# Optimization experiments

Measured on AMD Instinct MI355X. Metric: run time of the kernel, lower is better.

The kernel has to match this reference:

```python
import jax, jax.numpy as jnp
import numpy as np

NSAMPLE = 1024   # FPS centroids S
NGROUP = 32      # neighbors per ball K
RADIUS = 0.2


def _sqdist(a, b):
    # a: [B,S,3], b: [B,N,3] -> [B,S,N] squared euclidean distances
    return (jnp.sum(a * a, -1)[:, :, None]
            + jnp.sum(b * b, -1)[:, None, :]
            - 2.0 * jnp.einsum('bsc,bnc->bsn', a, b))


def farthest_point_sample(xyz, npoint):
    # xyz: [B,N,3] -> indices [B,npoint]. Deterministic start at index 0
    # (torch version randomizes the first centroid).
    B, N, _ = xyz.shape

    def step(carry, _):
        distance, farthest = carry
        centroid = jnp.take_along_axis(xyz, farthest[:, None, None], axis=1)  # [B,1,3]
        d = jnp.sum((xyz - centroid) ** 2, -1)                                 # [B,N]
        distance = jnp.minimum(distance, d)
        new_far = jnp.argmax(distance, -1).astype(jnp.int32)
        return (distance, new_far), farthest

    init = (jnp.full((B, N), 1e10, xyz.dtype), jnp.zeros((B,), jnp.int32))
    _, cents = jax.lax.scan(step, init, None, length=npoint)  # [npoint,B]
    return cents.T  # [B,npoint]


def query_ball_point(radius, nsample, xyz, new_xyz):
    # xyz: [B,N,3], new_xyz: [B,S,3] -> int idx [B,S,nsample]
    B, N, _ = xyz.shape
    sqr = _sqdist(new_xyz, xyz)                       # [B,S,N]
    idx = jnp.broadcast_to(jnp.arange(N, dtype=jnp.int32), sqr.shape)
    idx = jnp.where(sqr > radius * radius, N, idx)    # invalid -> sentinel N
    idx = jnp.sort(idx, axis=-1)[:, :, :nsample]      # smallest valid indices first
    first = idx[:, :, :1]
    idx = jnp.where(idx == N, first, idx)             # pad with first neighbor
    return idx.astype(jnp.int32)


def _gather_points(points, idx):
    # points: [B,N,C], idx: [B,S,K] -> [B,S,K,C]
    return jax.vmap(lambda p, i: p[i])(points, idx)


def setup_inputs() -> dict:
    key = jax.random.key(0)
    ks = jax.random.split(key, 8)
    B, N, D = 16, 8192, 64
    xyz = jax.random.uniform(ks[0], (B, N, 3), dtype=jnp.float32)
    points_fea = jax.random.normal(ks[1], (B, N, D), dtype=jnp.float32)
    s = 0.05
    W1 = jax.random.normal(ks[2], (67, 64), dtype=jnp.float32) * s
    b1 = jnp.zeros((64,), jnp.float32)
    W2 = jax.random.normal(ks[3], (64, 128), dtype=jnp.float32) * s
    b2 = jnp.zeros((128,), jnp.float32)
    W3 = jax.random.normal(ks[4], (128, 256), dtype=jnp.float32) * s
    b3 = jnp.zeros((256,), jnp.float32)
    return {"xyz": xyz, "points_fea": points_fea, "W1": W1, "b1": b1,
            "W2": W2, "b2": b2, "W3": W3, "b3": b3}


def reference(xyz, points_fea, W1, b1, W2, b2, W3, b3):
    # --- sample_and_group (fps + ball query) ---
    fps_idx = farthest_point_sample(xyz, NSAMPLE)                       # [B,S]
    sampled_xyz = jnp.take_along_axis(xyz, fps_idx[..., None], axis=1)  # [B,S,3]
    grouped_idx = query_ball_point(RADIUS, NGROUP, xyz, sampled_xyz)    # [B,S,K]
    grouped_xyz = _gather_points(xyz, grouped_idx)                      # [B,S,K,3]
    rel = grouped_xyz - sampled_xyz[:, :, None, :]
    grouped_fea = _gather_points(points_fea, grouped_idx)               # [B,S,K,D]
    feats = jnp.concatenate([rel, grouped_fea], axis=-1)                # [B,S,K,3+D]
    # --- per-point MLP (Linear+ReLU x3) ---
    h = jax.nn.relu(feats @ W1 + b1)
    h = jax.nn.relu(h @ W2 + b2)
    h = jax.nn.relu(h @ W3 + b3)                                        # [B,S,K,256]
    # --- max-pool over neighbors ---
    out = jnp.max(h, axis=2)                                            # [B,S,256]
    return sampled_xyz, out
```

## Files before the change

### kernel.cpp

```cpp
#include <hip/hip_runtime.h>
#include <hip/hip_bf16.h>

#define N_PTS 8192
#define NSAMP 1024
#define NGRP  32

typedef __attribute__((ext_vector_type(8))) short bf16x8;
typedef __attribute__((ext_vector_type(4))) float f32x4;
typedef __attribute__((ext_vector_type(2))) float f32x2;

static __device__ inline unsigned short f2bf(float f) {
  __hip_bfloat16 h = __float2bfloat16(f);
  return __builtin_bit_cast(unsigned short, h);
}

#define DPP_MAXSTEP(r, ctrl)                                                  \
  r = fmaxf(r, __int_as_float(__builtin_amdgcn_update_dpp(                    \
          __float_as_int(r), __float_as_int(r), (ctrl), 0xf, 0xf, false)))

#define FINAL8(P, V, F) do {                                                  \
    const uint4* pp_ = (const uint4*)&(P)[0];                                 \
    uint4 p0_ = pp_[0], p1_ = pp_[1], p2_ = pp_[2], p3_ = pp_[3];             \
    V = __uint_as_float(p0_.x); F = p0_.y;                                    \
    float q_;                                                                 \
    q_ = __uint_as_float(p0_.z); if (q_ > V) { V = q_; F = p0_.w; }           \
    q_ = __uint_as_float(p1_.x); if (q_ > V) { V = q_; F = p1_.y; }           \
    q_ = __uint_as_float(p1_.z); if (q_ > V) { V = q_; F = p1_.w; }           \
    q_ = __uint_as_float(p2_.x); if (q_ > V) { V = q_; F = p2_.y; }           \
    q_ = __uint_as_float(p2_.z); if (q_ > V) { V = q_; F = p2_.w; }           \
    q_ = __uint_as_float(p3_.x); if (q_ > V) { V = q_; F = p3_.y; }           \
    q_ = __uint_as_float(p3_.z); if (q_ > V) { V = q_; F = p3_.w; }           \
  } while (0)

static __device__ inline void load16(const float* __restrict__ bx, int t,
                                     float px[16], float py[16], float pz[16]) {
  const float4* src = (const float4*)(bx + t * 48);
  float4 v0 = src[0], v1 = src[1], v2 = src[2];
  float4 v3 = src[3], v4 = src[4], v5 = src[5];
  float4 v6 = src[6], v7 = src[7], v8 = src[8];
  float4 v9 = src[9], v10 = src[10], v11 = src[11];
  px[ 0]=v0.x; py[ 0]=v0.y; pz[ 0]=v0.z;
  px[ 1]=v0.w; py[ 1]=v1.x; pz[ 1]=v1.y;
  px[ 2]=v1.z; py[ 2]=v1.w; pz[ 2]=v2.x;
  px[ 3]=v2.y; py[ 3]=v2.z; pz[ 3]=v2.w;
  px[ 4]=v3.x; py[ 4]=v3.y; pz[ 4]=v3.z;
  px[ 5]=v3.w; py[ 5]=v4.x; pz[ 5]=v4.y;
  px[ 6]=v4.z; py[ 6]=v4.w; pz[ 6]=v5.x;
  px[ 7]=v5.y; py[ 7]=v5.z; pz[ 7]=v5.w;
  px[ 8]=v6.x; py[ 8]=v6.y; pz[ 8]=v6.z;
  px[ 9]=v6.w; py[ 9]=v7.x; pz[ 9]=v7.y;
  px[10]=v7.z; py[10]=v7.w; pz[10]=v8.x;
  px[11]=v8.y; py[11]=v8.z; pz[11]=v8.w;
  px[12]=v9.x; py[12]=v9.y; pz[12]=v9.z;
  px[13]=v9.w; py[13]=v10.x; pz[13]=v10.y;
  px[14]=v10.z; py[14]=v10.w; pz[14]=v11.x;
  px[15]=v11.y; py[15]=v11.z; pz[15]=v11.w;
}

__global__
__attribute__((amdgpu_flat_work_group_size(512, 512)))
__attribute__((amdgpu_waves_per_eu(2, 2)))
void fps_kernel(
    const float* __restrict__ xyz, float* __restrict__ out_sampled)
{
  #pragma clang fp contract(off)
  const int b = blockIdx.x;
  const int t = threadIdx.x;
  const float* bx = xyz + (size_t)b * N_PTS * 3;

  float px[16], py[16], pz[16];
  load16(bx, t, px, py, pz);

  f32x2 px2[8], py2[8], pz2[8], ds2[8];
  #pragma unroll
  for (int j = 0; j < 8; ++j) {
    px2[j] = (f32x2){px[2*j], px[2*j+1]};
    py2[j] = (f32x2){py[2*j], py[2*j+1]};
    pz2[j] = (f32x2){pz[2*j], pz[2*j+1]};
    ds2[j] = (f32x2){10000000000.0f, 10000000000.0f};
  }

  __shared__ float lds_p[N_PTS * 3];
  __shared__ float out_lds[NSAMP * 3];
  __shared__ __align__(16) uint2 part[2][8];

  for (int i = t; i < N_PTS * 3; i += 512) lds_p[i] = bx[i];

  const int lane = t & 63;
  const int wv   = t >> 6;

  float cx = bx[0], cy = bx[1], cz = bx[2];

  for (int it = 0; it < NSAMP; ++it) {
    if (t == 0) {
      out_lds[it * 3 + 0] = cx;
      out_lds[it * 3 + 1] = cy;
      out_lds[it * 3 + 2] = cz;
    }

    const f32x2 c2x = (f32x2){cx, cx};
    const f32x2 c2y = (f32x2){cy, cy};
    const f32x2 c2z = (f32x2){cz, cz};
    f32x2 bv2 = (f32x2){-1.0f, -1.0f};
    #pragma unroll
    for (int j = 0; j < 8; ++j) {
      f32x2 dx = px2[j] - c2x;
      f32x2 dy = py2[j] - c2y;
      f32x2 dz = pz2[j] - c2z;
      f32x2 d  = __builtin_elementwise_fma(
          dz, dz, __builtin_elementwise_fma(dy, dy, dx * dx));
      f32x2 nd = __builtin_elementwise_min(ds2[j], d);
      ds2[j] = nd;
      bv2 = __builtin_elementwise_max(bv2, nd);
    }
    float bv = fmaxf(bv2.x, bv2.y);

    int bi = t * 16 + 15;
    #pragma unroll
    for (int r = 14; r >= 0; --r) {
      float dr = (r & 1) ? ds2[r >> 1].y : ds2[r >> 1].x;
      bi = (dr == bv) ? (t * 16 + r) : bi;
    }

    float rmax = bv;
    DPP_MAXSTEP(rmax, 0x111);
    DPP_MAXSTEP(rmax, 0x112);
    DPP_MAXSTEP(rmax, 0x114);
    DPP_MAXSTEP(rmax, 0x118);
    DPP_MAXSTEP(rmax, 0x142);
    DPP_MAXSTEP(rmax, 0x143);
    float vmax = __int_as_float(
        __builtin_amdgcn_readlane(__float_as_int(rmax), 63));

    unsigned long long m = __ballot(bv == vmax);
    int L = __ffsll((long long)m) - 1;
    int widx = __builtin_amdgcn_readlane(bi, L);

    const int slot = it & 1;
    if (lane == 0) part[slot][wv] = make_uint2(__float_as_uint(vmax), (unsigned)widx);
    __syncthreads();

    float v; unsigned f;
    FINAL8(part[slot], v, f);

    cx = lds_p[f * 3 + 0];
    cy = lds_p[f * 3 + 1];
    cz = lds_p[f * 3 + 2];
  }

  __syncthreads();
  float* ob = out_sampled + (size_t)b * NSAMP * 3;
  for (int i = t; i < NSAMP * 3; i += 512) ob[i] = out_lds[i];
}

__global__ __launch_bounds__(256) void ball_kernel(
    const float* __restrict__ xyz, const float* __restrict__ sampled,
    int* __restrict__ gidx)
{
  #pragma clang fp contract(off)
  const float R2 = (float)(0.2 * 0.2);
  int gt = blockIdx.x * 256 + threadIdx.x;
  int w = gt >> 6;
  int lane = gt & 63;
  const int b = w >> 10;
  const float* cp = sampled + (size_t)w * 3;
  float cx = cp[0], cy = cp[1], cz = cp[2];
  float na = ((cx * cx) + (cy * cy)) + (cz * cz);
  const float* bx = xyz + (size_t)b * N_PTS * 3;
  int* out = gidx + (size_t)w * NGRP;

  int cnt = 0;
  int first = 0;
  for (int base = 0; base < N_PTS && cnt < NGRP; base += 64) {
    int p = base + lane;
    float x = bx[p * 3 + 0];
    float y = bx[p * 3 + 1];
    float z = bx[p * 3 + 2];
    float nb  = ((x * x) + (y * y)) + (z * z);
    float dot = fmaf(cz, z, fmaf(cy, y, cx * x));
    float sq  = (na + nb) - (2.0f * dot);
    bool inr = !(sq > R2);
    unsigned long long m = __ballot(inr);
    if (cnt == 0 && m != 0ull) first = base + (__ffsll(m) - 1);
    int before = __popcll(m & ((1ull << lane) - 1ull));
    int pos = cnt + before;
    if (inr && pos < NGRP) out[pos] = p;
    cnt += __popcll(m);
  }
  if (cnt < NGRP) {
    int q = cnt + lane;
    if (q < NGRP) out[q] = first;
  }
}

__global__ __launch_bounds__(256) void prep_w_kernel(
    const float* __restrict__ W1, const float* __restrict__ W2,
    const float* __restrict__ W3, unsigned short* __restrict__ wf1,
    unsigned short* __restrict__ wf2, unsigned short* __restrict__ wf3)
{
  int tid = blockIdx.x * 256 + threadIdx.x;
  int rec = tid >> 6, lane = tid & 63;
  if (rec >= 92) return;
  const float* W; unsigned short* dst; int N, K, ksteps, rl; int permuted;
  if (rec < 12)      { W = W1; dst = wf1; N = 64;  K = 67;  ksteps = 3; rl = rec;     permuted = 1; }
  else if (rec < 28) { W = W2; dst = wf2; N = 128; K = 64;  ksteps = 2; rl = rec - 12; permuted = 0; }
  else               { W = W3; dst = wf3; N = 256; K = 128; ksteps = 4; rl = rec - 28; permuted = 0; }
  int nt = rl / ksteps, ks = rl - nt * ksteps;
  int n  = nt * 16 + (lane & 15);
  int kb = ks * 32 + (lane >> 4) * 8;
  unsigned short v[8] __attribute__((aligned(16)));
  #pragma unroll
  for (int j = 0; j < 8; ++j) {
    int k = kb + j;
    float val;
    if (permuted) {
      if (k < 64)      val = W[(k + 3) * N + n];
      else if (k < K)  val = W[(k - 64) * N + n];
      else             val = 0.0f;
    } else {
      val = (k < K) ? W[k * N + n] : 0.0f;
    }
    v[j] = f2bf(val);
  }
  *(uint4*)(dst + ((size_t)rl * 64 + lane) * 8) = *(const uint4*)v;
}

__global__ __launch_bounds__(256, 4) void mlp_mfma_kernel(
    const float* __restrict__ xyz, const float* __restrict__ fea,
    const float* __restrict__ sampled, const int* __restrict__ gidx,
    const unsigned short* __restrict__ wf1, const unsigned short* __restrict__ wf2,
    const unsigned short* __restrict__ wf3, const float* __restrict__ b1,
    const float* __restrict__ b2, const float* __restrict__ b3,
    float* __restrict__ out)
{
  __shared__ __align__(16) unsigned short fT[32][104];
  __shared__ __align__(16) unsigned short h1[32][72];
  __shared__ __align__(16) unsigned short h2[32][136];
  __shared__ float pmax[8][256];
  __shared__ int   sidx[32];
  __shared__ float sc[4];

  const int bs = blockIdx.x;
  const int b  = bs >> 10;
  const int t  = threadIdx.x;
  const int w    = t >> 6;
  const int lane = t & 63;
  const int quad = lane >> 4;
  const int ncol = lane & 15;

  if (t < 32) sidx[t] = gidx[(size_t)bs * 32 + t];
  if (t < 3)  sc[t] = sampled[(size_t)bs * 3 + t];
  __syncthreads();

  {
    const int pt = t >> 3, c0 = t & 7;
    const int p = sidx[pt];
    const float4* fp4 = (const float4*)(fea + ((size_t)b * N_PTS + p) * 64);

    float4 fa = fp4[c0];
    float4 fb = fp4[c0 + 8];
    unsigned short sa[4] __attribute__((aligned(8)));
    unsigned short sb[4] __attribute__((aligned(8)));
    sa[0] = f2bf(fa.x); sa[1] = f2bf(fa.y); sa[2] = f2bf(fa.z); sa[3] = f2bf(fa.w);
    sb[0] = f2bf(fb.x); sb[1] = f2bf(fb.y); sb[2] = f2bf(fb.z); sb[3] = f2bf(fb.w);
    *(uint2*)&fT[pt][c0 * 4]      = *(const uint2*)sa;
    *(uint2*)&fT[pt][32 + c0 * 4] = *(const uint2*)sb;

    if (c0 == 0) {
      const float* xp = xyz + ((size_t)b * N_PTS + p) * 3;
      unsigned short sr[4] __attribute__((aligned(8)));
      sr[0] = f2bf(xp[0] - sc[0]);
      sr[1] = f2bf(xp[1] - sc[1]);
      sr[2] = f2bf(xp[2] - sc[2]);
      sr[3] = 0;
      *(uint2*)&fT[pt][64] = *(const uint2*)sr;
      *(uint2*)&fT[pt][68] = (uint2){0u, 0u};
    } else if (c0 >= 4 && c0 <= 6) {
      *(uint4*)&fT[pt][72 + (c0 - 4) * 8] = (uint4){0u, 0u, 0u, 0u};
    }
  }
  __syncthreads();

  #pragma unroll
  for (int q2 = 0; q2 < 2; ++q2) {
    const int tid = w * 2 + q2, mt = tid & 1, nt = tid >> 1;
    float bb = b1[nt * 16 + ncol];
    f32x4 acc = {bb, bb, bb, bb};
    #pragma unroll
    for (int ks = 0; ks < 3; ++ks) {
      bf16x8 a = *(const bf16x8*)&fT[mt * 16 + ncol][ks * 32 + quad * 8];
      bf16x8 bf = *(const bf16x8*)(wf1 + ((size_t)(nt * 3 + ks) * 64 + lane) * 8);
      acc = __builtin_amdgcn_mfma_f32_16x16x32_bf16(a, bf, acc, 0, 0, 0);
    }
    #pragma unroll
    for (int r = 0; r < 4; ++r)
      h1[mt * 16 + quad * 4 + r][nt * 16 + ncol] = f2bf(fmaxf(acc[r], 0.0f));
  }
  __syncthreads();

  #pragma unroll
  for (int q2 = 0; q2 < 4; ++q2) {
    const int tid = w * 4 + q2, mt = tid & 1, nt = tid >> 1;
    float bb = b2[nt * 16 + ncol];
    f32x4 acc = {bb, bb, bb, bb};
    #pragma unroll
    for (int ks = 0; ks < 2; ++ks) {
      bf16x8 a = *(const bf16x8*)&h1[mt * 16 + ncol][ks * 32 + quad * 8];
      bf16x8 bf = *(const bf16x8*)(wf2 + ((size_t)(nt * 2 + ks) * 64 + lane) * 8);
      acc = __builtin_amdgcn_mfma_f32_16x16x32_bf16(a, bf, acc, 0, 0, 0);
    }
    #pragma unroll
    for (int r = 0; r < 4; ++r)
      h2[mt * 16 + quad * 4 + r][nt * 16 + ncol] = f2bf(fmaxf(acc[r], 0.0f));
  }
  __syncthreads();

  #pragma unroll
  for (int q2 = 0; q2 < 8; ++q2) {
    const int tid = w * 8 + q2, mt = tid & 1, nt = tid >> 1;
    float bb = b3[nt * 16 + ncol];
    f32x4 acc = {bb, bb, bb, bb};
    #pragma unroll
    for (int ks = 0; ks < 4; ++ks) {
      bf16x8 a = *(const bf16x8*)&h2[mt * 16 + ncol][ks * 32 + quad * 8];
      bf16x8 bf = *(const bf16x8*)(wf3 + ((size_t)(nt * 4 + ks) * 64 + lane) * 8);
      acc = __builtin_amdgcn_mfma_f32_16x16x32_bf16(a, bf, acc, 0, 0, 0);
    }
    float mx = fmaxf(fmaxf(acc[0], acc[1]), fmaxf(acc[2], acc[3]));
    pmax[mt * 4 + quad][nt * 16 + ncol] = mx;
  }
  __syncthreads();

  {
    float v = pmax[0][t];
    #pragma unroll
    for (int s = 1; s < 8; ++s) v = fmaxf(v, pmax[s][t]);
    out[(size_t)bs * 256 + t] = fmaxf(v, 0.0f);
  }
}

extern "C" void kernel_launch(void* const* d_in, const int* in_sizes, int n_in,
                              void* d_out, int out_size, void* d_ws, size_t ws_size,
                              hipStream_t stream) {
  const float* xyz = (const float*)d_in[0];
  const float* fea = (const float*)d_in[1];
  const float* W1  = (const float*)d_in[2];
  const float* b1  = (const float*)d_in[3];
  const float* W2  = (const float*)d_in[4];
  const float* b2  = (const float*)d_in[5];
  const float* W3  = (const float*)d_in[6];
  const float* b3  = (const float*)d_in[7];

  float* outp    = (float*)d_out;
  float* sampled = outp;
  float* mlp_out = outp + 16 * 1024 * 3;
  int*   gidx    = (int*)d_ws;
  unsigned short* wf1 = (unsigned short*)((char*)d_ws + (2u << 20));
  unsigned short* wf2 = wf1 + (size_t)12 * 64 * 8;
  unsigned short* wf3 = wf2 + (size_t)16 * 64 * 8;

  fps_kernel<<<16, 512, 0, stream>>>(xyz, sampled);
  prep_w_kernel<<<23, 256, 0, stream>>>(W1, W2, W3, wf1, wf2, wf3);
  ball_kernel<<<4096, 256, 0, stream>>>(xyz, sampled, gidx);
  mlp_mfma_kernel<<<16384, 256, 0, stream>>>(xyz, fea, sampled, gidx,
                                             wf1, wf2, wf3, b1, b2, b3, mlp_out);
}
```

Measured before the change: 1.034 ms.

## Process two centroids per MLP block with register-tiled MFMA and shuffle max-pool

Each MLP block now handles two sampled centroids (64 grouped points), and each wave computes a full column tile across all four row tiles. This reuses every weight fragment load for four MFMAs, and the final layer reuses A fragments across two column tiles. The max-pool now uses in-register reductions and cross-lane shuffles instead of a shared-memory pmax array and an extra barrier. Block indices are swizzled across batches. The cost is more accumulator registers per thread and half as many blocks, while the overall runtime still includes FPS and ball query, which are untouched.

```diff
diff --git a/kernel.cpp b/kernel.cpp
--- a/kernel.cpp
+++ b/kernel.cpp
@@ -233,109 +233,145 @@
     const float* __restrict__ b2, const float* __restrict__ b3,
     float* __restrict__ out)
 {
-  __shared__ __align__(16) unsigned short fT[32][104];
-  __shared__ __align__(16) unsigned short h1[32][72];
-  __shared__ __align__(16) unsigned short h2[32][136];
-  __shared__ float pmax[8][256];
-  __shared__ int   sidx[32];
-  __shared__ float sc[4];
-
-  const int bs = blockIdx.x;
-  const int b  = bs >> 10;
-  const int t  = threadIdx.x;
+  __shared__ __align__(16) unsigned short fT[64][104];
+  __shared__ __align__(16) unsigned short h1[64][72];
+  __shared__ __align__(16) unsigned short h2[64][136];
+  __shared__ int   sidx[64];
+  __shared__ float sc[8];
+
+  const int wk  = (blockIdx.x & 7) * 1024 + (blockIdx.x >> 3);
+  const int bs0 = wk * 2;
+  const int b   = bs0 >> 10;
+  const int t   = threadIdx.x;
   const int w    = t >> 6;
   const int lane = t & 63;
   const int quad = lane >> 4;
   const int ncol = lane & 15;
 
-  if (t < 32) sidx[t] = gidx[(size_t)bs * 32 + t];
-  if (t < 3)  sc[t] = sampled[(size_t)bs * 3 + t];
+  if (t < 64) sidx[t] = gidx[(size_t)bs0 * 32 + t];
+  if (t < 6)  sc[t] = sampled[(size_t)bs0 * 3 + t];
   __syncthreads();
 
   {
-    const int pt = t >> 3, c0 = t & 7;
+    const int pt = t >> 2, c0 = t & 3;
     const int p = sidx[pt];
     const float4* fp4 = (const float4*)(fea + ((size_t)b * N_PTS + p) * 64);
-
-    float4 fa = fp4[c0];
-    float4 fb = fp4[c0 + 8];
-    unsigned short sa[4] __attribute__((aligned(8)));
-    unsigned short sb[4] __attribute__((aligned(8)));
-    sa[0] = f2bf(fa.x); sa[1] = f2bf(fa.y); sa[2] = f2bf(fa.z); sa[3] = f2bf(fa.w);
-    sb[0] = f2bf(fb.x); sb[1] = f2bf(fb.y); sb[2] = f2bf(fb.z); sb[3] = f2bf(fb.w);
-    *(uint2*)&fT[pt][c0 * 4]      = *(const uint2*)sa;
-    *(uint2*)&fT[pt][32 + c0 * 4] = *(const uint2*)sb;
-
+    #pragma unroll
+    for (int j = 0; j < 4; ++j) {
+      float4 fv = fp4[c0 + 4 * j];
+      unsigned short s4[4] __attribute__((aligned(8)));
+      s4[0] = f2bf(fv.x); s4[1] = f2bf(fv.y);
+      s4[2] = f2bf(fv.z); s4[3] = f2bf(fv.w);
+      *(uint2*)&fT[pt][(c0 + 4 * j) * 4] = *(const uint2*)s4;
+    }
     if (c0 == 0) {
       const float* xp = xyz + ((size_t)b * N_PTS + p) * 3;
+      const int cc = (pt >> 5) * 3;
       unsigned short sr[4] __attribute__((aligned(8)));
-      sr[0] = f2bf(xp[0] - sc[0]);
-      sr[1] = f2bf(xp[1] - sc[1]);
-      sr[2] = f2bf(xp[2] - sc[2]);
+      sr[0] = f2bf(xp[0] - sc[cc + 0]);
+      sr[1] = f2bf(xp[1] - sc[cc + 1]);
+      sr[2] = f2bf(xp[2] - sc[cc + 2]);
       sr[3] = 0;
       *(uint2*)&fT[pt][64] = *(const uint2*)sr;
       *(uint2*)&fT[pt][68] = (uint2){0u, 0u};
-    } else if (c0 >= 4 && c0 <= 6) {
-      *(uint4*)&fT[pt][72 + (c0 - 4) * 8] = (uint4){0u, 0u, 0u, 0u};
+    } else {
+      *(uint4*)&fT[pt][72 + (c0 - 1) * 8] = (uint4){0u, 0u, 0u, 0u};
     }
   }
   __syncthreads();
 
+  {
+    const int nt = w;
+    float bb = b1[nt * 16 + ncol];
+    f32x4 acc[4];
+    #pragma unroll
+    for (int mt = 0; mt < 4; ++mt) acc[mt] = (f32x4){bb, bb, bb, bb};
+    #pragma unroll
+    for (int ks = 0; ks < 3; ++ks) {
+      bf16x8 bf = *(const bf16x8*)(wf1 + ((size_t)(nt * 3 + ks) * 64 + lane) * 8);
+      #pragma unroll
+      for (int mt = 0; mt < 4; ++mt) {
+        bf16x8 a = *(const bf16x8*)&fT[mt * 16 + ncol][ks * 32 + quad * 8];
+        acc[mt] = __builtin_amdgcn_mfma_f32_16x16x32_bf16(a, bf, acc[mt], 0, 0, 0);
+      }
+    }
+    #pragma unroll
+    for (int mt = 0; mt < 4; ++mt)
+      #pragma unroll
+      for (int r = 0; r < 4; ++r)
+        h1[mt * 16 + quad * 4 + r][nt * 16 + ncol] = f2bf(fmaxf(acc[mt][r], 0.0f));
+  }
+  __syncthreads();
+
   #pragma unroll
-  for (int q2 = 0; q2 < 2; ++q2) {
-    const int tid = w * 2 + q2, mt = tid & 1, nt = tid >> 1;
-    float bb = b1[nt * 16 + ncol];
-    f32x4 acc = {bb, bb, bb, bb};
-    #pragma unroll
-    for (int ks = 0; ks < 3; ++ks) {
-      bf16x8 a = *(const bf16x8*)&fT[mt * 16 + ncol][ks * 32 + quad * 8];
-      bf16x8 bf = *(const bf16x8*)(wf1 + ((size_t)(nt * 3 + ks) * 64 + lane) * 8);
-      acc = __builtin_amdgcn_mfma_f32_16x16x32_bf16(a, bf, acc, 0, 0, 0);
-    }
-    #pragma unroll
-    for (int r = 0; r < 4; ++r)
-      h1[mt * 16 + quad * 4 + r][nt * 16 + ncol] = f2bf(fmaxf(acc[r], 0.0f));
+  for (int i = 0; i < 2; ++i) {
+    const int nt = 2 * w + i;
+    float bb = b2[nt * 16 + ncol];
+    f32x4 acc[4];
+    #pragma unroll
+    for (int mt = 0; mt < 4; ++mt) acc[mt] = (f32x4){bb, bb, bb, bb};
+    #pragma unroll
+    for (int ks = 0; ks < 2; ++ks) {
+      bf16x8 bf = *(const bf16x8*)(wf2 + ((size_t)(nt * 2 + ks) * 64 + lane) * 8);
+      #pragma unroll
+      for (int mt = 0; mt < 4; ++mt) {
+        bf16x8 a = *(const bf16x8*)&h1[mt * 16 + ncol][ks * 32 + quad * 8];
+        acc[mt] = __builtin_amdgcn_mfma_f32_16x16x32_bf16(a, bf, acc[mt], 0, 0, 0);
+      }
+    }
+    #pragma unroll
+    for (int mt = 0; mt < 4; ++mt)
+      #pragma unroll
+      for (int r = 0; r < 4; ++r)
+        h2[mt * 16 + quad * 4 + r][nt * 16 + ncol] = f2bf(fmaxf(acc[mt][r], 0.0f));
   }
   __syncthreads();
 
   #pragma unroll
-  for (int q2 = 0; q2 < 4; ++q2) {
-    const int tid = w * 4 + q2, mt = tid & 1, nt = tid >> 1;
-    float bb = b2[nt * 16 + ncol];
-    f32x4 acc = {bb, bb, bb, bb};
-    #pragma unroll
-    for (int ks = 0; ks < 2; ++ks) {
-      bf16x8 a = *(const bf16x8*)&h1[mt * 16 + ncol][ks * 32 + quad * 8];
-      bf16x8 bf = *(const bf16x8*)(wf2 + ((size_t)(nt * 2 + ks) * 64 + lane) * 8);
-      acc = __builtin_amdgcn_mfma_f32_16x16x32_bf16(a, bf, acc, 0, 0, 0);
-    }
-    #pragma unroll
-    for (int r = 0; r < 4; ++r)
-      h2[mt * 16 + quad * 4 + r][nt * 16 + ncol] = f2bf(fmaxf(acc[r], 0.0f));
-  }
-  __syncthreads();
-
-  #pragma unroll
-  for (int q2 = 0; q2 < 8; ++q2) {
-    const int tid = w * 8 + q2, mt = tid & 1, nt = tid >> 1;
-    float bb = b3[nt * 16 + ncol];
-    f32x4 acc = {bb, bb, bb, bb};
+  for (int half = 0; half < 2; ++half) {
+    f32x4 acc[2][4];
+    #pragma unroll
+    for (int i = 0; i < 2; ++i) {
+      const int nt = 4 * w + half * 2 + i;
+      float bb = b3[nt * 16 + ncol];
+      #pragma unroll
+      for (int mt = 0; mt < 4; ++mt) acc[i][mt] = (f32x4){bb, bb, bb, bb};
+    }
     #pragma unroll
     for (int ks = 0; ks < 4; ++ks) {
-      bf16x8 a = *(const bf16x8*)&h2[mt * 16 + ncol][ks * 32 + quad * 8];
-      bf16x8 bf = *(const bf16x8*)(wf3 + ((size_t)(nt * 4 + ks) * 64 + lane) * 8);
-      acc = __builtin_amdgcn_mfma_f32_16x16x32_bf16(a, bf, acc, 0, 0, 0);
-    }
-    float mx = fmaxf(fmaxf(acc[0], acc[1]), fmaxf(acc[2], acc[3]));
-    pmax[mt * 4 + quad][nt * 16 + ncol] = mx;
-  }
-  __syncthreads();
-
-  {
-    float v = pmax[0][t];
-    #pragma unroll
-    for (int s = 1; s < 8; ++s) v = fmaxf(v, pmax[s][t]);
-    out[(size_t)bs * 256 + t] = fmaxf(v, 0.0f);
+      bf16x8 a[4];
+      #pragma unroll
+      for (int mt = 0; mt < 4; ++mt)
+        a[mt] = *(const bf16x8*)&h2[mt * 16 + ncol][ks * 32 + quad * 8];
+      #pragma unroll
+      for (int i = 0; i < 2; ++i) {
+        const int nt = 4 * w + half * 2 + i;
+        bf16x8 bf = *(const bf16x8*)(wf3 + ((size_t)(nt * 4 + ks) * 64 + lane) * 8);
+        #pragma unroll
+        for (int mt = 0; mt < 4; ++mt)
+          acc[i][mt] = __builtin_amdgcn_mfma_f32_16x16x32_bf16(a[mt], bf, acc[i][mt], 0, 0, 0);
+      }
+    }
+    #pragma unroll
+    for (int i = 0; i < 2; ++i) {
+      const int nt = 4 * w + half * 2 + i;
+      float m0 = fmaxf(fmaxf(acc[i][0][0], acc[i][0][1]),
+                       fmaxf(acc[i][0][2], acc[i][0][3]));
+      m0 = fmaxf(m0, fmaxf(fmaxf(acc[i][1][0], acc[i][1][1]),
+                           fmaxf(acc[i][1][2], acc[i][1][3])));
+      float m1 = fmaxf(fmaxf(acc[i][2][0], acc[i][2][1]),
+                       fmaxf(acc[i][2][2], acc[i][2][3]));
+      m1 = fmaxf(m1, fmaxf(fmaxf(acc[i][3][0], acc[i][3][1]),
+                           fmaxf(acc[i][3][2], acc[i][3][3])));
+      m0 = fmaxf(m0, __shfl_xor(m0, 16));
+      m0 = fmaxf(m0, __shfl_xor(m0, 32));
+      m1 = fmaxf(m1, __shfl_xor(m1, 16));
+      m1 = fmaxf(m1, __shfl_xor(m1, 32));
+      if (quad == 0)
+        out[(size_t)bs0 * 256 + nt * 16 + ncol] = fmaxf(m0, 0.0f);
+      else if (quad == 1)
+        out[(size_t)(bs0 + 1) * 256 + nt * 16 + ncol] = fmaxf(m1, 0.0f);
+    }
   }
 }
 
@@ -362,6 +398,6 @@
   fps_kernel<<<16, 512, 0, stream>>>(xyz, sampled);
   prep_w_kernel<<<23, 256, 0, stream>>>(W1, W2, W3, wf1, wf2, wf3);
   ball_kernel<<<4096, 256, 0, stream>>>(xyz, sampled, gidx);
-  mlp_mfma_kernel<<<16384, 256, 0, stream>>>(xyz, fea, sampled, gidx,
-                                             wf1, wf2, wf3, b1, b2, b3, mlp_out);
-}
+  mlp_mfma_kernel<<<8192, 256, 0, stream>>>(xyz, fea, sampled, gidx,
+                                            wf1, wf2, wf3, b1, b2, b3, mlp_out);
+}
```

Result: no change. 1.014 ms (-1.9%).

## Fuse FPS, ball query and MLP into a persistent kernel with progress flags

Applied to the files above, without the earlier changes.

Replaces the four launches with one persistent kernel. Sixteen blocks run farthest-point sampling and publish progress every 128 samples. The remaining worker blocks convert the weights, then each wave handles whole centroids: ball query, gather and the three-layer MFMA MLP, with the max-pool done by shuffles. This lets the ball query and MLP run alongside the serial FPS instead of after it, and removes the gidx round trip and most block-level barriers. The cost is spin-waiting on global atomics, a deadlock risk if the FPS blocks are not co-resident, and less parallelism per centroid.

```diff
diff --git a/kernel.cpp b/kernel.cpp
--- a/kernel.cpp
+++ b/kernel.cpp
@@ -4,6 +4,8 @@
 #define N_PTS 8192
 #define NSAMP 1024
 #define NGRP  32
+#define NWORK_BLK 224
+#define NWAVES (NWORK_BLK * 8)
 
 typedef __attribute__((ext_vector_type(8))) short bf16x8;
 typedef __attribute__((ext_vector_type(4))) float f32x4;
@@ -57,285 +59,310 @@
   px[15]=v11.y; py[15]=v11.z; pz[15]=v11.w;
 }
 
+struct WaveBuf {
+  unsigned short fT[32][104];
+  unsigned short h1[32][72];
+  unsigned short h2[32][136];
+  int idx[32];
+};
+
+union SMemU {
+  struct {
+    float lds_p[N_PTS * 3];
+    float out_lds[NSAMP * 3];
+    uint2 part[2][8];
+  } f;
+  struct {
+    WaveBuf wb[8];
+  } w;
+};
+
 __global__
 __attribute__((amdgpu_flat_work_group_size(512, 512)))
 __attribute__((amdgpu_waves_per_eu(2, 2)))
-void fps_kernel(
-    const float* __restrict__ xyz, float* __restrict__ out_sampled)
+void mega_kernel(
+    const float* __restrict__ xyz, const float* __restrict__ fea,
+    const float* __restrict__ W1, const float* __restrict__ W2,
+    const float* __restrict__ W3, const float* __restrict__ b1,
+    const float* __restrict__ b2, const float* __restrict__ b3,
+    unsigned short* __restrict__ wf1, unsigned short* __restrict__ wf2,
+    unsigned short* __restrict__ wf3, float* __restrict__ sampled,
+    float* __restrict__ mlp_out, int* __restrict__ ctrl)
 {
   #pragma clang fp contract(off)
-  const int b = blockIdx.x;
-  const int t = threadIdx.x;
-  const float* bx = xyz + (size_t)b * N_PTS * 3;
-
-  float px[16], py[16], pz[16];
-  load16(bx, t, px, py, pz);
-
-  f32x2 px2[8], py2[8], pz2[8], ds2[8];
-  #pragma unroll
-  for (int j = 0; j < 8; ++j) {
-    px2[j] = (f32x2){px[2*j], px[2*j+1]};
-    py2[j] = (f32x2){py[2*j], py[2*j+1]};
-    pz2[j] = (f32x2){pz[2*j], pz[2*j+1]};
-    ds2[j] = (f32x2){10000000000.0f, 10000000000.0f};
-  }
-
-  __shared__ float lds_p[N_PTS * 3];
-  __shared__ float out_lds[NSAMP * 3];
-  __shared__ __align__(16) uint2 part[2][8];
-
-  for (int i = t; i < N_PTS * 3; i += 512) lds_p[i] = bx[i];
-
+  __shared__ __align__(16) SMemU sm;
+  const int t    = threadIdx.x;
   const int lane = t & 63;
   const int wv   = t >> 6;
-
-  float cx = bx[0], cy = bx[1], cz = bx[2];
-
-  for (int it = 0; it < NSAMP; ++it) {
-    if (t == 0) {
-      out_lds[it * 3 + 0] = cx;
-      out_lds[it * 3 + 1] = cy;
-      out_lds[it * 3 + 2] = cz;
-    }
-
-    const f32x2 c2x = (f32x2){cx, cx};
-    const f32x2 c2y = (f32x2){cy, cy};
-    const f32x2 c2z = (f32x2){cz, cz};
-    f32x2 bv2 = (f32x2){-1.0f, -1.0f};
+  int* progress = ctrl;
+  int* wdone    = ctrl + 16;
+
+  if (blockIdx.x < 16) {
+    const int b = blockIdx.x;
+    const float* bx = xyz + (size_t)b * N_PTS * 3;
+    float* ob = sampled + (size_t)b * NSAMP * 3;
+
+    float px[16], py[16], pz[16];
+    load16(bx, t, px, py, pz);
+
+    f32x2 px2[8], py2[8], pz2[8], ds2[8];
     #pragma unroll
     for (int j = 0; j < 8; ++j) {
-      f32x2 dx = px2[j] - c2x;
-      f32x2 dy = py2[j] - c2y;
-      f32x2 dz = pz2[j] - c2z;
-      f32x2 d  = __builtin_elementwise_fma(
-          dz, dz, __builtin_elementwise_fma(dy, dy, dx * dx));
-      f32x2 nd = __builtin_elementwise_min(ds2[j], d);
-      ds2[j] = nd;
-      bv2 = __builtin_elementwise_max(bv2, nd);
-    }
-    float bv = fmaxf(bv2.x, bv2.y);
-
-    int bi = t * 16 + 15;
-    #pragma unroll
-    for (int r = 14; r >= 0; --r) {
-      float dr = (r & 1) ? ds2[r >> 1].y : ds2[r >> 1].x;
-      bi = (dr == bv) ? (t * 16 + r) : bi;
-    }
-
-    float rmax = bv;
-    DPP_MAXSTEP(rmax, 0x111);
-    DPP_MAXSTEP(rmax, 0x112);
-    DPP_MAXSTEP(rmax, 0x114);
-    DPP_MAXSTEP(rmax, 0x118);
-    DPP_MAXSTEP(rmax, 0x142);
-    DPP_MAXSTEP(rmax, 0x143);
-    float vmax = __int_as_float(
-        __builtin_amdgcn_readlane(__float_as_int(rmax), 63));
-
-    unsigned long long m = __ballot(bv == vmax);
-    int L = __ffsll((long long)m) - 1;
-    int widx = __builtin_amdgcn_readlane(bi, L);
-
-    const int slot = it & 1;
-    if (lane == 0) part[slot][wv] = make_uint2(__float_as_uint(vmax), (unsigned)widx);
+      px2[j] = (f32x2){px[2*j], px[2*j+1]};
+      py2[j] = (f32x2){py[2*j], py[2*j+1]};
+      pz2[j] = (f32x2){pz[2*j], pz[2*j+1]};
+      ds2[j] = (f32x2){10000000000.0f, 10000000000.0f};
+    }
+
+    for (int i = t; i < N_PTS * 3; i += 512) sm.f.lds_p[i] = bx[i];
+
+    float cx = bx[0], cy = bx[1], cz = bx[2];
+
+    for (int it = 0; it < NSAMP; ++it) {
+      if ((it & 127) == 0 && it != 0) {
+        if (t < 96) {
+          float4 v = *(const float4*)&sm.f.out_lds[(it - 128) * 3 + t * 4];
+          *(float4*)&ob[(it - 128) * 3 + t * 4] = v;
+        }
+      }
+      if ((it & 127) == 64 && it > 64 && t == 0) {
+        __hip_atomic_store(&progress[b], it - 64, __ATOMIC_RELEASE,
+                           __HIP_MEMORY_SCOPE_AGENT);
+      }
+      if (t == 0) {
+        sm.f.out_lds[it * 3 + 0] = cx;
+        sm.f.out_lds[it * 3 + 1] = cy;
+        sm.f.out_lds[it * 3 + 2] = cz;
+      }
+
+      const f32x2 c2x = (f32x2){cx, cx};
+      const f32x2 c2y = (f32x2){cy, cy};
+      const f32x2 c2z = (f32x2){cz, cz};
+      f32x2 bv2 = (f32x2){-1.0f, -1.0f};
+      #pragma unroll
+      for (int j = 0; j < 8; ++j) {
+        f32x2 dx = px2[j] - c2x;
+        f32x2 dy = py2[j] - c2y;
+        f32x2 dz = pz2[j] - c2z;
+        f32x2 d  = __builtin_elementwise_fma(
+            dz, dz, __builtin_elementwise_fma(dy, dy, dx * dx));
+        f32x2 nd = __builtin_elementwise_min(ds2[j], d);
+        ds2[j] = nd;
+        bv2 = __builtin_elementwise_max(bv2, nd);
+      }
+      float bv = fmaxf(bv2.x, bv2.y);
+
+      int bi = t * 16 + 15;
+      #pragma unroll
+      for (int r = 14; r >= 0; --r) {
+        float dr = (r & 1) ? ds2[r >> 1].y : ds2[r >> 1].x;
+        bi = (dr == bv) ? (t * 16 + r) : bi;
+      }
+
+      float rmax = bv;
+      DPP_MAXSTEP(rmax, 0x111);
+      DPP_MAXSTEP(rmax, 0x112);
+      DPP_MAXSTEP(rmax, 0x114);
+      DPP_MAXSTEP(rmax, 0x118);
+      DPP_MAXSTEP(rmax, 0x142);
+      DPP_MAXSTEP(rmax, 0x143);
+      float vmax = __int_as_float(
+          __builtin_amdgcn_readlane(__float_as_int(rmax), 63));
+
+      unsigned long long m = __ballot(bv == vmax);
+      int L = __ffsll((long long)m) - 1;
+      int widx = __builtin_amdgcn_readlane(bi, L);
+
+      const int slot = it & 1;
+      if (lane == 0)
+        sm.f.part[slot][wv] = make_uint2(__float_as_uint(vmax), (unsigned)widx);
+      __syncthreads();
+
+      float v; unsigned f;
+      FINAL8(sm.f.part[slot], v, f);
+
+      cx = sm.f.lds_p[f * 3 + 0];
+      cy = sm.f.lds_p[f * 3 + 1];
+      cz = sm.f.lds_p[f * 3 + 2];
+    }
+
+    if (t < 96) {
+      float4 v = *(const float4*)&sm.f.out_lds[(NSAMP - 128) * 3 + t * 4];
+      *(float4*)&ob[(NSAMP - 128) * 3 + t * 4] = v;
+    }
     __syncthreads();
-
-    float v; unsigned f;
-    FINAL8(part[slot], v, f);
-
-    cx = lds_p[f * 3 + 0];
-    cy = lds_p[f * 3 + 1];
-    cz = lds_p[f * 3 + 2];
+    if (t == 0)
+      __hip_atomic_store(&progress[b], NSAMP, __ATOMIC_RELEASE,
+                         __HIP_MEMORY_SCOPE_AGENT);
+    return;
   }
 
-  __syncthreads();
-  float* ob = out_sampled + (size_t)b * NSAMP * 3;
-  for (int i = t; i < NSAMP * 3; i += 512) ob[i] = out_lds[i];
-}
-
-__global__ __launch_bounds__(256) void ball_kernel(
-    const float* __restrict__ xyz, const float* __restrict__ sampled,
-    int* __restrict__ gidx)
-{
-  #pragma clang fp contract(off)
-  const float R2 = (float)(0.2 * 0.2);
-  int gt = blockIdx.x * 256 + threadIdx.x;
-  int w = gt >> 6;
-  int lane = gt & 63;
-  const int b = w >> 10;
-  const float* cp = sampled + (size_t)w * 3;
-  float cx = cp[0], cy = cp[1], cz = cp[2];
-  float na = ((cx * cx) + (cy * cy)) + (cz * cz);
-  const float* bx = xyz + (size_t)b * N_PTS * 3;
-  int* out = gidx + (size_t)w * NGRP;
-
-  int cnt = 0;
-  int first = 0;
-  for (int base = 0; base < N_PTS && cnt < NGRP; base += 64) {
-    int p = base + lane;
-    float x = bx[p * 3 + 0];
-    float y = bx[p * 3 + 1];
-    float z = bx[p * 3 + 2];
-    float nb  = ((x * x) + (y * y)) + (z * z);
-    float dot = fmaf(cz, z, fmaf(cy, y, cx * x));
-    float sq  = (na + nb) - (2.0f * dot);
-    bool inr = !(sq > R2);
-    unsigned long long m = __ballot(inr);
-    if (cnt == 0 && m != 0ull) first = base + (__ffsll(m) - 1);
-    int before = __popcll(m & ((1ull << lane) - 1ull));
-    int pos = cnt + before;
-    if (inr && pos < NGRP) out[pos] = p;
-    cnt += __popcll(m);
-  }
-  if (cnt < NGRP) {
-    int q = cnt + lane;
-    if (q < NGRP) out[q] = first;
-  }
-}
-
-__global__ __launch_bounds__(256) void prep_w_kernel(
-    const float* __restrict__ W1, const float* __restrict__ W2,
-    const float* __restrict__ W3, unsigned short* __restrict__ wf1,
-    unsigned short* __restrict__ wf2, unsigned short* __restrict__ wf3)
-{
-  int tid = blockIdx.x * 256 + threadIdx.x;
-  int rec = tid >> 6, lane = tid & 63;
-  if (rec >= 92) return;
-  const float* W; unsigned short* dst; int N, K, ksteps, rl; int permuted;
-  if (rec < 12)      { W = W1; dst = wf1; N = 64;  K = 67;  ksteps = 3; rl = rec;     permuted = 1; }
-  else if (rec < 28) { W = W2; dst = wf2; N = 128; K = 64;  ksteps = 2; rl = rec - 12; permuted = 0; }
-  else               { W = W3; dst = wf3; N = 256; K = 128; ksteps = 4; rl = rec - 28; permuted = 0; }
-  int nt = rl / ksteps, ks = rl - nt * ksteps;
-  int n  = nt * 16 + (lane & 15);
-  int kb = ks * 32 + (lane >> 4) * 8;
-  unsigned short v[8] __attribute__((aligned(16)));
-  #pragma unroll
-  for (int j = 0; j < 8; ++j) {
-    int k = kb + j;
-    float val;
-    if (permuted) {
-      if (k < 64)      val = W[(k + 3) * N + n];
-      else if (k < K)  val = W[(k - 64) * N + n];
-      else             val = 0.0f;
-    } else {
-      val = (k < K) ? W[k * N + n] : 0.0f;
-    }
-    v[j] = f2bf(val);
-  }
-  *(uint4*)(dst + ((size_t)rl * 64 + lane) * 8) = *(const uint4*)v;
-}
-
-__global__ __launch_bounds__(256, 4) void mlp_mfma_kernel(
-    const float* __restrict__ xyz, const float* __restrict__ fea,
-    const float* __restrict__ sampled, const int* __restrict__ gidx,
-    const unsigned short* __restrict__ wf1, const unsigned short* __restrict__ wf2,
-    const unsigned short* __restrict__ wf3, const float* __restrict__ b1,
-    const float* __restrict__ b2, const float* __restrict__ b3,
-    float* __restrict__ out)
-{
-  __shared__ __align__(16) unsigned short fT[32][104];
-  __shared__ __align__(16) unsigned short h1[32][72];
-  __shared__ __align__(16) unsigned short h2[32][136];
-  __shared__ float pmax[8][256];
-  __shared__ int   sidx[32];
-  __shared__ float sc[4];
-
-  const int bs = blockIdx.x;
-  const int b  = bs >> 10;
-  const int t  = threadIdx.x;
-  const int w    = t >> 6;
-  const int lane = t & 63;
+  const int wbk = blockIdx.x - 16;
   const int quad = lane >> 4;
   const int ncol = lane & 15;
-
-  if (t < 32) sidx[t] = gidx[(size_t)bs * 32 + t];
-  if (t < 3)  sc[t] = sampled[(size_t)bs * 3 + t];
-  __syncthreads();
-
-  {
-    const int pt = t >> 3, c0 = t & 7;
-    const int p = sidx[pt];
-    const float4* fp4 = (const float4*)(fea + ((size_t)b * N_PTS + p) * 64);
-
-    float4 fa = fp4[c0];
-    float4 fb = fp4[c0 + 8];
-    unsigned short sa[4] __attribute__((aligned(8)));
-    unsigned short sb[4] __attribute__((aligned(8)));
-    sa[0] = f2bf(fa.x); sa[1] = f2bf(fa.y); sa[2] = f2bf(fa.z); sa[3] = f2bf(fa.w);
-    sb[0] = f2bf(fb.x); sb[1] = f2bf(fb.y); sb[2] = f2bf(fb.z); sb[3] = f2bf(fb.w);
-    *(uint2*)&fT[pt][c0 * 4]      = *(const uint2*)sa;
-    *(uint2*)&fT[pt][32 + c0 * 4] = *(const uint2*)sb;
-
-    if (c0 == 0) {
-      const float* xp = xyz + ((size_t)b * N_PTS + p) * 3;
-      unsigned short sr[4] __attribute__((aligned(8)));
-      sr[0] = f2bf(xp[0] - sc[0]);
-      sr[1] = f2bf(xp[1] - sc[1]);
-      sr[2] = f2bf(xp[2] - sc[2]);
-      sr[3] = 0;
-      *(uint2*)&fT[pt][64] = *(const uint2*)sr;
-      *(uint2*)&fT[pt][68] = (uint2){0u, 0u};
-    } else if (c0 >= 4 && c0 <= 6) {
-      *(uint4*)&fT[pt][72 + (c0 - 4) * 8] = (uint4){0u, 0u, 0u, 0u};
-    }
+  const float R2 = (float)(0.2 * 0.2);
+
+  if (wbk < 12) {
+    int tid = wbk * 512 + t;
+    int rec = tid >> 6, plane = tid & 63;
+    if (rec < 92) {
+      const float* W; unsigned short* dst; int N, K, ksteps, rl; int permuted;
+      if (rec < 12)      { W = W1; dst = wf1; N = 64;  K = 67;  ksteps = 3; rl = rec;      permuted = 1; }
+      else if (rec < 28) { W = W2; dst = wf2; N = 128; K = 64;  ksteps = 2; rl = rec - 12; permuted = 0; }
+      else               { W = W3; dst = wf3; N = 256; K = 128; ksteps = 4; rl = rec - 28; permuted = 0; }
+      int nt = rl / ksteps, ks = rl - nt * ksteps;
+      int n  = nt * 16 + (plane & 15);
+      int kb = ks * 32 + (plane >> 4) * 8;
+      unsigned short v[8] __attribute__((aligned(16)));
+      #pragma unroll
+      for (int j = 0; j < 8; ++j) {
+        int k = kb + j;
+        float val;
+        if (permuted) {
+          if (k < 64)      val = W[(k + 3) * N + n];
+          else if (k < K)  val = W[(k - 64) * N + n];
+          else             val = 0.0f;
+        } else {
+          val = (k < K) ? W[k * N + n] : 0.0f;
+        }
+        v[j] = f2bf(val);
+      }
+      *(uint4*)(dst + ((size_t)rl * 64 + plane) * 8) = *(const uint4*)v;
+    }
+    __syncthreads();
+    if (t == 0)
+      __hip_atomic_fetch_add(wdone, 1, __ATOMIC_RELEASE,
+                             __HIP_MEMORY_SCOPE_AGENT);
   }
-  __syncthreads();
-
-  #pragma unroll
-  for (int q2 = 0; q2 < 2; ++q2) {
-    const int tid = w * 2 + q2, mt = tid & 1, nt = tid >> 1;
-    float bb = b1[nt * 16 + ncol];
-    f32x4 acc = {bb, bb, bb, bb};
+
+  while (__hip_atomic_load(wdone, __ATOMIC_ACQUIRE,
+                           __HIP_MEMORY_SCOPE_AGENT) < 12)
+    __builtin_amdgcn_s_sleep(8);
+
+  WaveBuf* Wb = &sm.w.wb[wv];
+  const int gw = wbk * 8 + wv;
+
+  for (int item = gw; item < 16 * NSAMP; item += NWAVES) {
+    const int si = item >> 4;
+    const int b  = item & 15;
+    const int sg = b * NSAMP + si;
+
+    while (__hip_atomic_load(&progress[b], __ATOMIC_ACQUIRE,
+                             __HIP_MEMORY_SCOPE_AGENT) <= si)
+      __builtin_amdgcn_s_sleep(32);
+
+    const float* cp = sampled + (size_t)sg * 3;
+    float cx = cp[0], cy = cp[1], cz = cp[2];
+    float na = ((cx * cx) + (cy * cy)) + (cz * cz);
+    const float* bx = xyz + (size_t)b * N_PTS * 3;
+
+    int cnt = 0, first = 0;
+    for (int base = 0; base < N_PTS && cnt < NGRP; base += 64) {
+      int p = base + lane;
+      float x = bx[p * 3 + 0];
+      float y = bx[p * 3 + 1];
+      float z = bx[p * 3 + 2];
+      float nb  = ((x * x) + (y * y)) + (z * z);
+      float dot = fmaf(cz, z, fmaf(cy, y, cx * x));
+      float sq  = (na + nb) - (2.0f * dot);
+      bool inr = !(sq > R2);
+      unsigned long long m = __ballot(inr);
+      if (cnt == 0 && m != 0ull) first = base + (__ffsll(m) - 1);
+      int before = __popcll(m & ((1ull << lane) - 1ull));
+      int pos = cnt + before;
+      if (inr && pos < NGRP) Wb->idx[pos] = p;
+      cnt += __popcll(m);
+    }
+    if (cnt < NGRP) {
+      int q = cnt + lane;
+      if (q < NGRP) Wb->idx[q] = first;
+    }
+
+    {
+      const int pt = lane >> 1, c0 = lane & 1;
+      const int p = Wb->idx[pt];
+      const float4* fp4 = (const float4*)(fea + ((size_t)b * N_PTS + p) * 64);
+      #pragma unroll
+      for (int j = 0; j < 8; ++j) {
+        float4 fv = fp4[c0 + 2 * j];
+        unsigned short s4[4] __attribute__((aligned(8)));
+        s4[0] = f2bf(fv.x); s4[1] = f2bf(fv.y);
+        s4[2] = f2bf(fv.z); s4[3] = f2bf(fv.w);
+        *(uint2*)&Wb->fT[pt][(c0 + 2 * j) * 4] = *(const uint2*)s4;
+      }
+      if (c0 == 0) {
+        const float* xp = xyz + ((size_t)b * N_PTS + p) * 3;
+        unsigned short sr[4] __attribute__((aligned(8)));
+        sr[0] = f2bf(xp[0] - cx);
+        sr[1] = f2bf(xp[1] - cy);
+        sr[2] = f2bf(xp[2] - cz);
+        sr[3] = 0;
+        *(uint2*)&Wb->fT[pt][64] = *(const uint2*)sr;
+        *(uint2*)&Wb->fT[pt][68] = (uint2){0u, 0u};
+      } else {
+        *(uint4*)&Wb->fT[pt][72] = (uint4){0u, 0u, 0u, 0u};
+        *(uint4*)&Wb->fT[pt][80] = (uint4){0u, 0u, 0u, 0u};
+        *(uint4*)&Wb->fT[pt][88] = (uint4){0u, 0u, 0u, 0u};
+      }
+    }
+
     #pragma unroll
-    for (int ks = 0; ks < 3; ++ks) {
-      bf16x8 a = *(const bf16x8*)&fT[mt * 16 + ncol][ks * 32 + quad * 8];
-      bf16x8 bf = *(const bf16x8*)(wf1 + ((size_t)(nt * 3 + ks) * 64 + lane) * 8);
-      acc = __builtin_amdgcn_mfma_f32_16x16x32_bf16(a, bf, acc, 0, 0, 0);
-    }
+    for (int nt = 0; nt < 4; ++nt) {
+      float bb = b1[nt * 16 + ncol];
+      f32x4 a0 = {bb, bb, bb, bb}, a1 = {bb, bb, bb, bb};
+      #pragma unroll
+      for (int ks = 0; ks < 3; ++ks) {
+        bf16x8 bf = *(const bf16x8*)(wf1 + ((size_t)(nt * 3 + ks) * 64 + lane) * 8);
+        bf16x8 f0 = *(const bf16x8*)&Wb->fT[ncol][ks * 32 + quad * 8];
+        bf16x8 f1 = *(const bf16x8*)&Wb->fT[16 + ncol][ks * 32 + quad * 8];
+        a0 = __builtin_amdgcn_mfma_f32_16x16x32_bf16(f0, bf, a0, 0, 0, 0);
+        a1 = __builtin_amdgcn_mfma_f32_16x16x32_bf16(f1, bf, a1, 0, 0, 0);
+      }
+      #pragma unroll
+      for (int r = 0; r < 4; ++r) {
+        Wb->h1[quad * 4 + r][nt * 16 + ncol]      = f2bf(fmaxf(a0[r], 0.0f));
+        Wb->h1[16 + quad * 4 + r][nt * 16 + ncol] = f2bf(fmaxf(a1[r], 0.0f));
+      }
+    }
+
     #pragma unroll
-    for (int r = 0; r < 4; ++r)
-      h1[mt * 16 + quad * 4 + r][nt * 16 + ncol] = f2bf(fmaxf(acc[r], 0.0f));
-  }
-  __syncthreads();
-
-  #pragma unroll
-  for (int q2 = 0; q2 < 4; ++q2) {
-    const int tid = w * 4 + q2, mt = tid & 1, nt = tid >> 1;
-    float bb = b2[nt * 16 + ncol];
-    f32x4 acc = {bb, bb, bb, bb};
+    for (int nt = 0; nt < 8; ++nt) {
+      float bb = b2[nt * 16 + ncol];
+      f32x4 a0 = {bb, bb, bb, bb}, a1 = {bb, bb, bb, bb};
+      #pragma unroll
+      for (int ks = 0; ks < 2; ++ks) {
+        bf16x8 bf = *(const bf16x8*)(wf2 + ((size_t)(nt * 2 + ks) * 64 + lane) * 8);
+        bf16x8 f0 = *(const bf16x8*)&Wb->h1[ncol][ks * 32 + quad * 8];
+        bf16x8 f1 = *(const bf16x8*)&Wb->h1[16 + ncol][ks * 32 + quad * 8];
+        a0 = __builtin_amdgcn_mfma_f32_16x16x32_bf16(f0, bf, a0, 0, 0, 0);
+        a1 = __builtin_amdgcn_mfma_f32_16x16x32_bf16(f1, bf, a1, 0, 0, 0);
+      }
+      #pragma unroll
+      for (int r = 0; r < 4; ++r) {
+        Wb->h2[quad * 4 + r][nt * 16 + ncol]      = f2bf(fmaxf(a0[r], 0.0f));
+        Wb->h2[16 + quad * 4 + r][nt * 16 + ncol] = f2bf(fmaxf(a1[r], 0.0f));
+      }
+    }
+
     #pragma unroll
-    for (int ks = 0; ks < 2; ++ks) {
-      bf16x8 a = *(const bf16x8*)&h1[mt * 16 + ncol][ks * 32 + quad * 8];
-      bf16x8 bf = *(const bf16x8*)(wf2 + ((size_t)(nt * 2 + ks) * 64 + lane) * 8);
-      acc = __builtin_amdgcn_mfma_f32_16x16x32_bf16(a, bf, acc, 0, 0, 0);
-    }
-    #pragma unroll
-    for (int r = 0; r < 4; ++r)
-      h2[mt * 16 + quad * 4 + r][nt * 16 + ncol] = f2bf(fmaxf(acc[r], 0.0f));
-  }
-  __syncthreads();
-
-  #pragma unroll
-  for (int q2 = 0; q2 < 8; ++q2) {
-    const int tid = w * 8 + q2, mt = tid & 1, nt = tid >> 1;
-    float bb = b3[nt * 16 + ncol];
-    f32x4 acc = {bb, bb, bb, bb};
-    #pragma unroll
-    for (int ks = 0; ks < 4; ++ks) {
-      bf16x8 a = *(const bf16x8*)&h2[mt * 16 + ncol][ks * 32 + quad * 8];
-      bf16x8 bf = *(const bf16x8*)(wf3 + ((size_t)(nt * 4 + ks) * 64 + lane) * 8);
-      acc = __builtin_amdgcn_mfma_f32_16x16x32_bf16(a, bf, acc, 0, 0, 0);
-    }
-    float mx = fmaxf(fmaxf(acc[0], acc[1]), fmaxf(acc[2], acc[3]));
-    pmax[mt * 4 + quad][nt * 16 + ncol] = mx;
-  }
-  __syncthreads();
-
-  {
-    float v = pmax[0][t];
-    #pragma unroll
-    for (int s = 1; s < 8; ++s) v = fmaxf(v, pmax[s][t]);
-    out[(size_t)bs * 256 + t] = fmaxf(v, 0.0f);
+    for (int nt = 0; nt < 16; ++nt) {
+      float bb = b3[nt * 16 + ncol];
+      f32x4 a0 = {bb, bb, bb, bb}, a1 = {bb, bb, bb, bb};
+      #pragma unroll
+      for (int ks = 0; ks < 4; ++ks) {
+        bf16x8 bf = *(const bf16x8*)(wf3 + ((size_t)(nt * 4 + ks) * 64 + lane) * 8);
+        bf16x8 f0 = *(const bf16x8*)&Wb->h2[ncol][ks * 32 + quad * 8];
+        bf16x8 f1 = *(const bf16x8*)&Wb->h2[16 + ncol][ks * 32 + quad * 8];
+        a0 = __builtin_amdgcn_mfma_f32_16x16x32_bf16(f0, bf, a0, 0, 0, 0);
+        a1 = __builtin_amdgcn_mfma_f32_16x16x32_bf16(f1, bf, a1, 0, 0, 0);
+      }
+      float mm = fmaxf(fmaxf(fmaxf(a0[0], a0[1]), fmaxf(a0[2], a0[3])),
+                       fmaxf(fmaxf(a1[0], a1[1]), fmaxf(a1[2], a1[3])));
+      mm = fmaxf(mm, __shfl_xor(mm, 16));
+      mm = fmaxf(mm, __shfl_xor(mm, 32));
+      if (quad == 0)
+        mlp_out[(size_t)sg * 256 + nt * 16 + ncol] = fmaxf(mm, 0.0f);
+    }
   }
 }
 
@@ -354,14 +381,14 @@
   float* outp    = (float*)d_out;
   float* sampled = outp;
   float* mlp_out = outp + 16 * 1024 * 3;
-  int*   gidx    = (int*)d_ws;
+
+  int* ctrl = (int*)d_ws;
   unsigned short* wf1 = (unsigned short*)((char*)d_ws + (2u << 20));
   unsigned short* wf2 = wf1 + (size_t)12 * 64 * 8;
   unsigned short* wf3 = wf2 + (size_t)16 * 64 * 8;
 
-  fps_kernel<<<16, 512, 0, stream>>>(xyz, sampled);
-  prep_w_kernel<<<23, 256, 0, stream>>>(W1, W2, W3, wf1, wf2, wf3);
-  ball_kernel<<<4096, 256, 0, stream>>>(xyz, sampled, gidx);
-  mlp_mfma_kernel<<<16384, 256, 0, stream>>>(xyz, fea, sampled, gidx,
-                                             wf1, wf2, wf3, b1, b2, b3, mlp_out);
+  hipMemsetAsync(ctrl, 0, 128, stream);
+  mega_kernel<<<16 + NWORK_BLK, 512, 0, stream>>>(
+      xyz, fea, W1, W2, W3, b1, b2, b3, wf1, wf2, wf3,
+      sampled, mlp_out, ctrl);
 }
```

After: 1.077 ms. 4.1% more time.
